# Kernel optimization log

Measured on AMD Instinct MI355X. Metric: run time of the kernel, lower is better.

Reference implementation:

```python
import jax, jax.numpy as jnp
import numpy as np

B, N, D, H, KS, DQ = 2048, 20, 512, 8, 3, 64
DK = D // H
LN_EPS = 1e-5


def _conv1d_same(x_bdn, w_oik):
    # x: [B, D, N], w: [O, I, K] -> [B, O, N], 'same' padding
    return jax.lax.conv_general_dilated(
        x_bdn, w_oik, window_strides=(1,), padding='SAME',
        dimension_numbers=('NCH', 'OIH', 'NCH'))


def _layernorm(x, g, b):
    m = jnp.mean(x, axis=-1, keepdims=True)
    v = jnp.var(x, axis=-1, keepdims=True)
    return (x - m) * jax.lax.rsqrt(v + LN_EPS) * g + b


def setup_inputs() -> dict:
    key = jax.random.key(0)
    ks = jax.random.split(key, 12)
    s = 0.02
    inp = {
        'x': jax.random.normal(ks[0], (B, N, D), dtype=jnp.float32),
        'Wq': jax.random.normal(ks[1], (D, D, KS), dtype=jnp.float32) * s,
        'Wk': jax.random.normal(ks[2], (D, D, KS), dtype=jnp.float32) * s,
        'Wv': jax.random.normal(ks[3], (D, D, KS), dtype=jnp.float32) * s,
        'gq_g': jnp.ones((D,), jnp.float32), 'gq_b': jnp.zeros((D,), jnp.float32),
        'gk_g': jnp.ones((D,), jnp.float32), 'gk_b': jnp.zeros((D,), jnp.float32),
        'gv_g': jnp.ones((D,), jnp.float32), 'gv_b': jnp.zeros((D,), jnp.float32),
        'rel_table': jax.random.normal(ks[4], (2 * N - 1, H), dtype=jnp.float32) * s,
        'gsb': jax.random.normal(ks[5], (H, N, N), dtype=jnp.float32) * s,
        'alpha': jnp.asarray(1.0, jnp.float32),
        'Wqf': jax.random.normal(ks[6], (D, DQ), dtype=jnp.float32) * s,
        'bqf': jnp.zeros((DQ,), jnp.float32),
        'Wqp': jax.random.normal(ks[7], (DQ, H), dtype=jnp.float32) * s,
        'bqp': jnp.zeros((H,), jnp.float32),
        'Wo': jax.random.normal(ks[8], (D, D), dtype=jnp.float32) * s,
        'bo': jnp.zeros((D,), jnp.float32),
    }
    return inp


def reference(x, Wq, Wk, Wv, gq_g, gq_b, gk_g, gk_b, gv_g, gv_b,
              rel_table, gsb, alpha, Wqf, bqf, Wqp, bqp, Wo, bo):
    xp = jnp.transpose(x, (0, 2, 1))  # [B, D, N]
    # conv QKV projections + LayerNorm + residual (use_conv_proj=True path)
    q = x + _layernorm(jnp.transpose(_conv1d_same(xp, Wq), (0, 2, 1)), gq_g, gq_b)
    k = x + _layernorm(jnp.transpose(_conv1d_same(xp, Wk), (0, 2, 1)), gk_g, gk_b)
    v = x + _layernorm(jnp.transpose(_conv1d_same(xp, Wv), (0, 2, 1)), gv_g, gv_b)
    # split heads: [B, H, N, DK]
    q = q.reshape(B, N, H, DK).transpose(0, 2, 1, 3)
    k = k.reshape(B, N, H, DK).transpose(0, 2, 1, 3)
    v = v.reshape(B, N, H, DK).transpose(0, 2, 1, 3)
    scale = 1.0 / jnp.sqrt(jnp.asarray(DK, jnp.float32))
    scores = jnp.einsum('bhnd,bhmd->bhnm', q, k) * scale  # [B, H, N, N]
    # relative positional bias over node index
    idx = jnp.arange(N)[:, None] - jnp.arange(N)[None, :] + N - 1  # [N, N]
    rel_bias = rel_table[idx]  # [N, N, H]
    scores = scores + jnp.transpose(rel_bias, (2, 0, 1))[None]
    # learned global spatial bias
    scores = scores + alpha * gsb[None]
    # dynamic adjacency bias from pairwise node features
    qf = jnp.tanh(x @ Wqf + bqf)  # [B, N, DQ]
    pair = qf[:, :, None, :] - qf[:, None, :, :]  # [B, N, N, DQ]
    dyn = pair @ Wqp + bqp  # [B, N, N, H]
    scores = scores + jnp.transpose(dyn, (0, 3, 1, 2))
    attn = jax.nn.softmax(scores, axis=-1)
    out = jnp.einsum('bhnm,bhmd->bhnd', attn, v)
    out = out.transpose(0, 2, 1, 3).reshape(B, N, D)
    return out @ Wo + bo
```

## Files before the change

kernel.cpp:

```cpp
#include <hip/hip_runtime.h>
#include <stdint.h>

#define Bn   2048
#define Nn   20
#define Dn   512
#define Hn   8
#define Mn   (Bn*Nn)
#define K3n  1536
#define NPn  22
#define BKn  32

typedef __attribute__((ext_vector_type(4))) float  floatx4;
typedef __attribute__((ext_vector_type(8))) __bf16 bf16x8;
typedef __attribute__((ext_vector_type(4))) __bf16 bf16x4;

__device__ __forceinline__ void gload_lds16(const void* g, void* l) {
  __builtin_amdgcn_global_load_lds(
      (const __attribute__((address_space(1))) void*)g,
      (__attribute__((address_space(3))) void*)l, 16, 0, 0);
}

__global__ void k_prep_xpad(const float* __restrict__ x, __bf16* __restrict__ xpad) {
  int idx = blockIdx.x * 256 + threadIdx.x;
  int d8 = idx & 63;
  int t  = idx >> 6;
  if (t >= Bn * NPn) return;
  int n = t % NPn;
  int b = t / NPn;
  bf16x8 v;
  if (n == 0 || n == NPn - 1) {
#pragma unroll
    for (int e = 0; e < 8; ++e) v[e] = (__bf16)0.f;
  } else {
    const float4 x0 = *(const float4*)(x + (size_t)((b * Nn + n - 1) * Dn) + d8 * 8);
    const float4 x1 = *(const float4*)(x + (size_t)((b * Nn + n - 1) * Dn) + d8 * 8 + 4);
    v[0] = (__bf16)x0.x; v[1] = (__bf16)x0.y; v[2] = (__bf16)x0.z; v[3] = (__bf16)x0.w;
    v[4] = (__bf16)x1.x; v[5] = (__bf16)x1.y; v[6] = (__bf16)x1.z; v[7] = (__bf16)x1.w;
  }
  *(bf16x8*)(xpad + (size_t)t * Dn + d8 * 8) = v;
}

__global__ void k_prep_wct(const float* __restrict__ Wq, const float* __restrict__ Wk,
                           const float* __restrict__ Wv, __bf16* __restrict__ wct) {
  int idx = blockIdx.x * 256 + threadIdx.x;
  if (idx >= K3n * K3n) return;
  int kk = idx % K3n;
  int j  = idx / K3n;
  int seg = j >> 9, o = j & 511;
  int kker = kk >> 9, i = kk & 511;
  const float* W = (seg == 0) ? Wq : ((seg == 1) ? Wk : Wv);
  wct[idx] = (__bf16)W[(o * 512 + i) * 3 + kker];
}

__global__ void k_prep_wot(const float* __restrict__ Wo, __bf16* __restrict__ wot) {
  int idx = blockIdx.x * 256 + threadIdx.x;
  if (idx >= Dn * Dn) return;
  int k = idx & 511, c = idx >> 9;
  wot[idx] = (__bf16)Wo[k * Dn + c];
}

__global__ void k_prep_wqft(const float* __restrict__ Wqf, __bf16* __restrict__ wqft) {
  int idx = blockIdx.x * 256 + threadIdx.x;
  if (idx >= Dn * 64) return;
  int d = idx & 511, dq = idx >> 9;
  wqft[idx] = (__bf16)Wqf[d * 64 + dq];
}

__global__ void k_bias(const float* __restrict__ rel, const float* __restrict__ gsb,
                       const float* __restrict__ alpha, const float* __restrict__ bqp,
                       float* __restrict__ bias) {
  int idx = blockIdx.x * 256 + threadIdx.x;
  if (idx >= Hn * Nn * Nn) return;
  int j = idx % Nn;
  int i = (idx / Nn) % Nn;
  int h = idx / (Nn * Nn);
  bias[idx] = rel[(i - j + Nn - 1) * Hn + h] + alpha[0] * gsb[idx] + bqp[h];
}

__global__ __launch_bounds__(512)
void k_qkv(const __bf16* __restrict__ xpad, const __bf16* __restrict__ wct,
           const float* __restrict__ gq_g, const float* __restrict__ gq_b,
           const float* __restrict__ gk_g, const float* __restrict__ gk_b,
           const float* __restrict__ gv_g, const float* __restrict__ gv_b,
           __bf16* __restrict__ qkv) {
  __shared__ __bf16 lA[64 * BKn];
  __shared__ __bf16 lB[512 * BKn];
  __shared__ float red1[256];
  __shared__ float red2[256];

  const int tid  = threadIdx.x;
  const int wave = tid >> 6;
  const int lane = tid & 63;
  const int quad = lane >> 4;
  const int l15  = lane & 15;
  const int rowg = wave >> 2;
  const int colg = wave & 3;

  const int bid   = blockIdx.x;
  const int xcd   = bid & 7;
  const int local = bid >> 3;
  const int seg   = local % 3;
  const int mt    = xcd * 80 + local / 3;
  const int m0    = mt * 64;

  const __bf16* gB[4];
#pragma unroll
  for (int t = 0; t < 4; ++t) {
    int c   = wave * 256 + t * 64 + lane;
    int col = c >> 2;
    int rk  = (c & 3) ^ ((col >> 1) & 3);
    gB[t] = wct + (size_t)(seg * 512 + col) * K3n + rk * 8;
  }
  const __bf16* gA;
  {
    int c   = (wave & 3) * 64 + lane;
    int row = c >> 2;
    int rk  = (c & 3) ^ ((row >> 1) & 3);
    int grow = m0 + row;
    int b = grow / Nn, n = grow - b * Nn;
    gA = xpad + (size_t)(b * NPn + n) * Dn + rk * 8;
  }

  const __bf16* fA[2];
#pragma unroll
  for (int tr = 0; tr < 2; ++tr) {
    int row  = rowg * 32 + tr * 16 + l15;
    int slot = quad ^ ((row >> 1) & 3);
    fA[tr] = lA + row * BKn + slot * 8;
  }
  const __bf16* fB[8];
#pragma unroll
  for (int tc = 0; tc < 8; ++tc) {
    int col  = colg * 128 + tc * 16 + l15;
    int slot = quad ^ ((col >> 1) & 3);
    fB[tc] = lB + col * BKn + slot * 8;
  }

  floatx4 acc[2][8];
  const floatx4 zero = {0.f, 0.f, 0.f, 0.f};
#pragma unroll
  for (int i = 0; i < 2; ++i)
#pragma unroll
    for (int j = 0; j < 8; ++j) acc[i][j] = zero;

  __bf16* dstB = lB + wave * 2048;
  __bf16* dstA = lA + (wave & 3) * 512;

  for (int kt = 0; kt < K3n / BKn; ++kt) {
#pragma unroll
    for (int t = 0; t < 4; ++t) gload_lds16(gB[t], dstB + t * 512);
    if (wave < 4) gload_lds16(gA, dstA);
    __syncthreads();
    bf16x8 a0 = *(const bf16x8*)fA[0];
    bf16x8 a1 = *(const bf16x8*)fA[1];
#pragma unroll
    for (int tc = 0; tc < 8; ++tc) {
      bf16x8 b0 = *(const bf16x8*)fB[tc];
      acc[0][tc] = __builtin_amdgcn_mfma_f32_16x16x32_bf16(a0, b0, acc[0][tc], 0, 0, 0);
      acc[1][tc] = __builtin_amdgcn_mfma_f32_16x16x32_bf16(a1, b0, acc[1][tc], 0, 0, 0);
    }
    __syncthreads();
#pragma unroll
    for (int t = 0; t < 4; ++t) gB[t] += BKn;
    gA += BKn;
  }

  float s1[8], s2[8];
#pragma unroll
  for (int tr = 0; tr < 2; ++tr)
#pragma unroll
    for (int r = 0; r < 4; ++r) {
      float a = 0.f, b2 = 0.f;
#pragma unroll
      for (int tc = 0; tc < 8; ++tc) { float v = acc[tr][tc][r]; a += v; b2 += v * v; }
      s1[tr * 4 + r] = a; s2[tr * 4 + r] = b2;
    }
#pragma unroll
  for (int off = 1; off < 16; off <<= 1)
#pragma unroll
    for (int i = 0; i < 8; ++i) {
      s1[i] += __shfl_xor(s1[i], off, 64);
      s2[i] += __shfl_xor(s2[i], off, 64);
    }
  if (l15 == 0) {
#pragma unroll
    for (int i = 0; i < 8; ++i) {
      int tr = i >> 2, r = i & 3;
      int row = rowg * 32 + tr * 16 + quad * 4 + r;
      red1[row * 4 + colg] = s1[i];
      red2[row * 4 + colg] = s2[i];
    }
  }
  __syncthreads();

  const float* gg = (seg == 0) ? gq_g : ((seg == 1) ? gk_g : gv_g);
  const float* bb = (seg == 0) ? gq_b : ((seg == 1) ? gk_b : gv_b);
#pragma unroll
  for (int tr = 0; tr < 2; ++tr)
#pragma unroll
    for (int r = 0; r < 4; ++r) {
      int row = rowg * 32 + tr * 16 + quad * 4 + r;
      float su = red1[row * 4] + red1[row * 4 + 1] + red1[row * 4 + 2] + red1[row * 4 + 3];
      float sq = red2[row * 4] + red2[row * 4 + 1] + red2[row * 4 + 2] + red2[row * 4 + 3];
      float m  = su * (1.f / 512.f);
      float vv = sq * (1.f / 512.f) - m * m;
      float rstd = rsqrtf(vv + 1e-5f);
      int grow = m0 + row;
      int b = grow / Nn, n2 = grow - b * Nn;
      const __bf16* xr = xpad + (size_t)(b * NPn + n2 + 1) * Dn;
#pragma unroll
      for (int tc = 0; tc < 8; ++tc) {
        int col = colg * 128 + tc * 16 + l15;
        float val = (acc[tr][tc][r] - m) * rstd * gg[col] + bb[col] + (float)xr[col];
        qkv[(size_t)grow * K3n + seg * 512 + col] = (__bf16)val;
      }
    }
}

__global__ __launch_bounds__(256)
void k_qfqp(const __bf16* __restrict__ xpad, const __bf16* __restrict__ wqft,
            const float* __restrict__ bqf, const float* __restrict__ wqp,
            float* __restrict__ qfp) {
  __shared__ __bf16 lA[64 * BKn];
  __shared__ __bf16 lB[64 * BKn];
  __shared__ float lWqpT[8 * 64];
  const int tid  = threadIdx.x;
  const int wave = tid >> 6;
  const int lane = tid & 63;
  const int quad = lane >> 4;
  const int l15  = lane & 15;
  const int m0   = blockIdx.x * 64;

#pragma unroll
  for (int t = tid; t < 512; t += 256) {
    int col = t & 63, h = t >> 6;
    lWqpT[t] = wqp[col * 8 + h];
  }

  int c = wave * 64 + lane;
  int rowc = c >> 2;
  int rk   = (c & 3) ^ ((rowc >> 1) & 3);
  int grow = m0 + rowc;
  int b = grow / Nn, n = grow - b * Nn;
  const __bf16* gA = xpad + (size_t)(b * NPn + n + 1) * Dn + rk * 8;
  const __bf16* gB = wqft + (size_t)rowc * Dn + rk * 8;

  int frow = wave * 16 + l15;
  const __bf16* fA = lA + frow * BKn + (quad ^ ((frow >> 1) & 3)) * 8;
  const __bf16* fB[4];
#pragma unroll
  for (int tc = 0; tc < 4; ++tc) {
    int col = tc * 16 + l15;
    fB[tc] = lB + col * BKn + (quad ^ ((col >> 1) & 3)) * 8;
  }

  const floatx4 zero = {0.f, 0.f, 0.f, 0.f};
  floatx4 acc[4] = {zero, zero, zero, zero};

  for (int kt = 0; kt < Dn / BKn; ++kt) {
    gload_lds16(gA, lA + wave * 512);
    gload_lds16(gB, lB + wave * 512);
    __syncthreads();
    bf16x8 a = *(const bf16x8*)fA;
#pragma unroll
    for (int tc = 0; tc < 4; ++tc)
      acc[tc] = __builtin_amdgcn_mfma_f32_16x16x32_bf16(a, *(const bf16x8*)fB[tc], acc[tc], 0, 0, 0);
    __syncthreads();
    gA += BKn; gB += BKn;
  }

  float part[4][8];
#pragma unroll
  for (int r = 0; r < 4; ++r)
#pragma unroll
    for (int h = 0; h < 8; ++h) part[r][h] = 0.f;
#pragma unroll
  for (int tc = 0; tc < 4; ++tc) {
    int col = tc * 16 + l15;
    float bq = bqf[col];
#pragma unroll
    for (int r = 0; r < 4; ++r) {
      float t = tanhf(acc[tc][r] + bq);
#pragma unroll
      for (int h = 0; h < 8; ++h) part[r][h] += t * lWqpT[h * 64 + col];
    }
  }
#pragma unroll
  for (int off = 1; off < 16; off <<= 1)
#pragma unroll
    for (int r = 0; r < 4; ++r)
#pragma unroll
      for (int h = 0; h < 8; ++h) part[r][h] += __shfl_xor(part[r][h], off, 64);
  if (l15 == 0) {
#pragma unroll
    for (int r = 0; r < 4; ++r) {
      int row = wave * 16 + quad * 4 + r;
#pragma unroll
      for (int h = 0; h < 8; ++h)
        qfp[(size_t)(m0 + row) * 8 + h] = part[r][h];
    }
  }
}

__global__ __launch_bounds__(256)
void k_attn(const __bf16* __restrict__ qkv, const float* __restrict__ qfp,
            const float* __restrict__ bias, __bf16* __restrict__ aout) {
  __shared__ float sq[4][Nn * 64];
  __shared__ float sk[4][Nn * 68];
  __shared__ float sv[4][Nn * 68];
  __shared__ float sp[4][Nn * Nn];
  __shared__ float sf[4][Nn];
  const int tid  = threadIdx.x;
  const int w    = tid >> 6;
  const int lane = tid & 63;
  const int p0 = blockIdx.x * 4 + w;
  const int b = p0 >> 3, h = p0 & 7;
  const __bf16* qb = qkv + (size_t)b * Nn * K3n + h * 64;

  for (int idx = lane; idx < 160; idx += 64) {
    int n = idx >> 3, c = (idx & 7) * 8;
    bf16x8 qv = *(const bf16x8*)(qb + (size_t)n * K3n + c);
    bf16x8 kv = *(const bf16x8*)(qb + (size_t)n * K3n + 512 + c);
    bf16x8 vv = *(const bf16x8*)(qb + (size_t)n * K3n + 1024 + c);
#pragma unroll
    for (int e = 0; e < 8; ++e) {
      sq[w][n * 64 + c + e] = (float)qv[e];
      sk[w][n * 68 + c + e] = (float)kv[e];
      sv[w][n * 68 + c + e] = (float)vv[e];
    }
  }
  if (lane < Nn) sf[w][lane] = qfp[(size_t)(b * Nn + lane) * 8 + h];
  __syncthreads();

  const float* bh = bias + h * Nn * Nn;
  for (int p = lane; p < Nn * Nn; p += 64) {
    int i = p / Nn, j = p - i * Nn;
    const float4* q4 = (const float4*)&sq[w][i * 64];
    const float4* k4 = (const float4*)&sk[w][j * 68];
    float s = 0.f;
#pragma unroll
    for (int d4 = 0; d4 < 16; ++d4) {
      float4 qa = q4[d4], ka = k4[d4];
      s += qa.x * ka.x + qa.y * ka.y + qa.z * ka.z + qa.w * ka.w;
    }
    sp[w][p] = s * 0.125f + bh[p] + sf[w][i] - sf[w][j];
  }
  __syncthreads();
  if (lane < Nn) {
    int i = lane;
    float* row = &sp[w][i * Nn];
    float mx = row[0];
    for (int j = 1; j < Nn; ++j) mx = fmaxf(mx, row[j]);
    float sum = 0.f;
    for (int j = 0; j < Nn; ++j) { float e = __expf(row[j] - mx); row[j] = e; sum += e; }
    float inv = 1.f / sum;
    for (int j = 0; j < Nn; ++j) row[j] *= inv;
  }
  __syncthreads();
  for (int i = 0; i < Nn; ++i) {
    float a = 0.f;
#pragma unroll
    for (int j = 0; j < Nn; ++j) a += sp[w][i * Nn + j] * sv[w][j * 68 + lane];
    aout[(size_t)(b * Nn + i) * Dn + h * 64 + lane] = (__bf16)a;
  }
}

__global__ __launch_bounds__(512)
void k_oproj(const __bf16* __restrict__ aout, const __bf16* __restrict__ wot,
             const float* __restrict__ bo, float* __restrict__ out) {
  __shared__ __bf16 lA[64 * BKn];
  __shared__ __bf16 lB[512 * BKn];
  const int tid  = threadIdx.x;
  const int wave = tid >> 6;
  const int lane = tid & 63;
  const int quad = lane >> 4;
  const int l15  = lane & 15;
  const int rowg = wave >> 2;
  const int colg = wave & 3;
  const int m0   = blockIdx.x * 64;

  const __bf16* gB[4];
#pragma unroll
  for (int t = 0; t < 4; ++t) {
    int c   = wave * 256 + t * 64 + lane;
    int col = c >> 2;
    int rk  = (c & 3) ^ ((col >> 1) & 3);
    gB[t] = wot + (size_t)col * Dn + rk * 8;
  }
  const __bf16* gA;
  {
    int c   = (wave & 3) * 64 + lane;
    int row = c >> 2;
    int rk  = (c & 3) ^ ((row >> 1) & 3);
    gA = aout + (size_t)(m0 + row) * Dn + rk * 8;
  }
  const __bf16* fA[2];
#pragma unroll
  for (int tr = 0; tr < 2; ++tr) {
    int row = rowg * 32 + tr * 16 + l15;
    fA[tr] = lA + row * BKn + (quad ^ ((row >> 1) & 3)) * 8;
  }
  const __bf16* fB[8];
#pragma unroll
  for (int tc = 0; tc < 8; ++tc) {
    int col = colg * 128 + tc * 16 + l15;
    fB[tc] = lB + col * BKn + (quad ^ ((col >> 1) & 3)) * 8;
  }

  const floatx4 zero = {0.f, 0.f, 0.f, 0.f};
  floatx4 acc[2][8];
#pragma unroll
  for (int i = 0; i < 2; ++i)
#pragma unroll
    for (int j = 0; j < 8; ++j) acc[i][j] = zero;

  __bf16* dstB = lB + wave * 2048;
  __bf16* dstA = lA + (wave & 3) * 512;

  for (int kt = 0; kt < Dn / BKn; ++kt) {
#pragma unroll
    for (int t = 0; t < 4; ++t) gload_lds16(gB[t], dstB + t * 512);
    if (wave < 4) gload_lds16(gA, dstA);
    __syncthreads();
    bf16x8 a0 = *(const bf16x8*)fA[0];
    bf16x8 a1 = *(const bf16x8*)fA[1];
#pragma unroll
    for (int tc = 0; tc < 8; ++tc) {
      bf16x8 b0 = *(const bf16x8*)fB[tc];
      acc[0][tc] = __builtin_amdgcn_mfma_f32_16x16x32_bf16(a0, b0, acc[0][tc], 0, 0, 0);
      acc[1][tc] = __builtin_amdgcn_mfma_f32_16x16x32_bf16(a1, b0, acc[1][tc], 0, 0, 0);
    }
    __syncthreads();
#pragma unroll
    for (int t = 0; t < 4; ++t) gB[t] += BKn;
    gA += BKn;
  }
#pragma unroll
  for (int tr = 0; tr < 2; ++tr)
#pragma unroll
    for (int r = 0; r < 4; ++r) {
      int row = rowg * 32 + tr * 16 + quad * 4 + r;
#pragma unroll
      for (int tc = 0; tc < 8; ++tc) {
        int col = colg * 128 + tc * 16 + l15;
        out[(size_t)(m0 + row) * Dn + col] = acc[tr][tc][r] + bo[col];
      }
    }
}

static const size_t OFF_XPAD = 0;
static const size_t OFF_WCT  = 46137344;
static const size_t OFF_WOT  = 50855936;
static const size_t OFF_WQFT = 51380224;
static const size_t OFF_QKV  = 51445760;
static const size_t OFF_QFP  = 177274880;
static const size_t OFF_BIAS = 178585600;
static const size_t OFF_AOUT = 0;

extern "C" void kernel_launch(void* const* d_in, const int* in_sizes, int n_in,
                              void* d_out, int out_size, void* d_ws, size_t ws_size,
                              hipStream_t stream) {
  (void)in_sizes; (void)n_in; (void)out_size; (void)ws_size;
  const float* x     = (const float*)d_in[0];
  const float* Wq    = (const float*)d_in[1];
  const float* Wk    = (const float*)d_in[2];
  const float* Wv    = (const float*)d_in[3];
  const float* gq_g  = (const float*)d_in[4];
  const float* gq_b  = (const float*)d_in[5];
  const float* gk_g  = (const float*)d_in[6];
  const float* gk_b  = (const float*)d_in[7];
  const float* gv_g  = (const float*)d_in[8];
  const float* gv_b  = (const float*)d_in[9];
  const float* rel   = (const float*)d_in[10];
  const float* gsb   = (const float*)d_in[11];
  const float* alpha = (const float*)d_in[12];
  const float* Wqf   = (const float*)d_in[13];
  const float* bqf   = (const float*)d_in[14];
  const float* Wqp   = (const float*)d_in[15];
  const float* bqp   = (const float*)d_in[16];
  const float* Wo    = (const float*)d_in[17];
  const float* bo    = (const float*)d_in[18];
  float* out = (float*)d_out;
  char* ws = (char*)d_ws;

  __bf16* xpad = (__bf16*)(ws + OFF_XPAD);
  __bf16* wct  = (__bf16*)(ws + OFF_WCT);
  __bf16* wot  = (__bf16*)(ws + OFF_WOT);
  __bf16* wqft = (__bf16*)(ws + OFF_WQFT);
  __bf16* qkv  = (__bf16*)(ws + OFF_QKV);
  float*  qfp  = (float*)(ws + OFF_QFP);
  float*  bias = (float*)(ws + OFF_BIAS);
  __bf16* aout = (__bf16*)(ws + OFF_AOUT);

  k_prep_xpad<<<(Bn * NPn * (Dn / 8) + 255) / 256, 256, 0, stream>>>(x, xpad);
  k_prep_wct <<<(K3n * K3n + 255) / 256, 256, 0, stream>>>(Wq, Wk, Wv, wct);
  k_prep_wot <<<(Dn * Dn + 255) / 256, 256, 0, stream>>>(Wo, wot);
  k_prep_wqft<<<(Dn * 64 + 255) / 256, 256, 0, stream>>>(Wqf, wqft);
  k_bias     <<<(Hn * Nn * Nn + 255) / 256, 256, 0, stream>>>(rel, gsb, alpha, bqp, bias);

  k_qkv <<<Mn / 64 * 3, 512, 0, stream>>>(xpad, wct, gq_g, gq_b, gk_g, gk_b, gv_g, gv_b, qkv);
  k_qfqp<<<Mn / 64, 256, 0, stream>>>(xpad, wqft, bqf, Wqp, qfp);
  k_attn<<<(Bn * Hn) / 4, 256, 0, stream>>>(qkv, qfp, bias, aout);
  k_oproj<<<Mn / 64, 512, 0, stream>>>(aout, wot, bo, out);
}
```

Measured before the change: 651.4 us.

## Triple-buffer QKV GEMM loads and double the M tile to 128

The fused conv-QKV GEMM now uses a 128-row M tile (4x8 MFMA tiles per wave), which halves the number of blocks and the redundant weight traffic per output row. It replaces the load/sync/compute loop with a three-stage LDS ring, so global-to-LDS loads for stage k+2 are issued before computing stage k, waited on with explicit vmcnt counters, and only one barrier per step remains. It also raises MFMA wave priority and asks for 2 blocks per CU via launch bounds. The costs are more LDS (about 120KB) and 128 accumulator registers per lane, which could limit occupancy or cause spills.

```diff
diff --git a/kernel.cpp b/kernel.cpp
--- a/kernel.cpp
+++ b/kernel.cpp
@@ -77,16 +77,15 @@
   bias[idx] = rel[(i - j + Nn - 1) * Hn + h] + alpha[0] * gsb[idx] + bqp[h];
 }
 
-__global__ __launch_bounds__(512)
+__global__ __launch_bounds__(512, 2)
 void k_qkv(const __bf16* __restrict__ xpad, const __bf16* __restrict__ wct,
            const float* __restrict__ gq_g, const float* __restrict__ gq_b,
            const float* __restrict__ gk_g, const float* __restrict__ gk_b,
            const float* __restrict__ gv_g, const float* __restrict__ gv_b,
            __bf16* __restrict__ qkv) {
-  __shared__ __bf16 lA[64 * BKn];
-  __shared__ __bf16 lB[512 * BKn];
-  __shared__ float red1[256];
-  __shared__ float red2[256];
+  __shared__ __bf16 lds[3 * 20480];
+  __shared__ float red1[512];
+  __shared__ float red2[512];
 
   const int tid  = threadIdx.x;
   const int wave = tid >> 6;
@@ -100,20 +99,24 @@
   const int xcd   = bid & 7;
   const int local = bid >> 3;
   const int seg   = local % 3;
-  const int mt    = xcd * 80 + local / 3;
-  const int m0    = mt * 64;
-
-  const __bf16* gB[4];
-#pragma unroll
-  for (int t = 0; t < 4; ++t) {
-    int c   = wave * 256 + t * 64 + lane;
-    int col = c >> 2;
-    int rk  = (c & 3) ^ ((col >> 1) & 3);
-    gB[t] = wct + (size_t)(seg * 512 + col) * K3n + rk * 8;
+  const int mt    = xcd * 40 + local / 3;
+  const int m0    = mt * 128;
+
+  const __bf16 *gB0, *gB1, *gB2, *gB3;
+  {
+    int c, col, rk;
+    c = wave * 256 + 0 * 64 + lane; col = c >> 2; rk = (c & 3) ^ ((col >> 1) & 3);
+    gB0 = wct + (size_t)(seg * 512 + col) * K3n + rk * 8;
+    c = wave * 256 + 1 * 64 + lane; col = c >> 2; rk = (c & 3) ^ ((col >> 1) & 3);
+    gB1 = wct + (size_t)(seg * 512 + col) * K3n + rk * 8;
+    c = wave * 256 + 2 * 64 + lane; col = c >> 2; rk = (c & 3) ^ ((col >> 1) & 3);
+    gB2 = wct + (size_t)(seg * 512 + col) * K3n + rk * 8;
+    c = wave * 256 + 3 * 64 + lane; col = c >> 2; rk = (c & 3) ^ ((col >> 1) & 3);
+    gB3 = wct + (size_t)(seg * 512 + col) * K3n + rk * 8;
   }
   const __bf16* gA;
   {
-    int c   = (wave & 3) * 64 + lane;
+    int c   = tid;
     int row = c >> 2;
     int rk  = (c & 3) ^ ((row >> 1) & 3);
     int grow = m0 + row;
@@ -121,72 +124,98 @@
     gA = xpad + (size_t)(b * NPn + n) * Dn + rk * 8;
   }
 
-  const __bf16* fA[2];
-#pragma unroll
-  for (int tr = 0; tr < 2; ++tr) {
-    int row  = rowg * 32 + tr * 16 + l15;
-    int slot = quad ^ ((row >> 1) & 3);
-    fA[tr] = lA + row * BKn + slot * 8;
-  }
-  const __bf16* fB[8];
-#pragma unroll
-  for (int tc = 0; tc < 8; ++tc) {
-    int col  = colg * 128 + tc * 16 + l15;
-    int slot = quad ^ ((col >> 1) & 3);
-    fB[tc] = lB + col * BKn + slot * 8;
-  }
-
-  floatx4 acc[2][8];
+  int fAo0, fAo1, fAo2, fAo3, fBo[8];
+  {
+    int row;
+    row = rowg * 64 + 0 * 16 + l15; fAo0 = row * BKn + (quad ^ ((row >> 1) & 3)) * 8;
+    row = rowg * 64 + 1 * 16 + l15; fAo1 = row * BKn + (quad ^ ((row >> 1) & 3)) * 8;
+    row = rowg * 64 + 2 * 16 + l15; fAo2 = row * BKn + (quad ^ ((row >> 1) & 3)) * 8;
+    row = rowg * 64 + 3 * 16 + l15; fAo3 = row * BKn + (quad ^ ((row >> 1) & 3)) * 8;
+#pragma unroll
+    for (int tc = 0; tc < 8; ++tc) {
+      int col = colg * 128 + tc * 16 + l15;
+      fBo[tc] = 4096 + col * BKn + (quad ^ ((col >> 1) & 3)) * 8;
+    }
+  }
+
+  const int dA = wave * 512;
+  const int dB = 4096 + wave * 2048;
+
+  floatx4 acc[4][8];
   const floatx4 zero = {0.f, 0.f, 0.f, 0.f};
 #pragma unroll
-  for (int i = 0; i < 2; ++i)
+  for (int i = 0; i < 4; ++i)
 #pragma unroll
     for (int j = 0; j < 8; ++j) acc[i][j] = zero;
 
-  __bf16* dstB = lB + wave * 2048;
-  __bf16* dstA = lA + (wave & 3) * 512;
-
-  for (int kt = 0; kt < K3n / BKn; ++kt) {
-#pragma unroll
-    for (int t = 0; t < 4; ++t) gload_lds16(gB[t], dstB + t * 512);
-    if (wave < 4) gload_lds16(gA, dstA);
-    __syncthreads();
-    bf16x8 a0 = *(const bf16x8*)fA[0];
-    bf16x8 a1 = *(const bf16x8*)fA[1];
-#pragma unroll
-    for (int tc = 0; tc < 8; ++tc) {
-      bf16x8 b0 = *(const bf16x8*)fB[tc];
-      acc[0][tc] = __builtin_amdgcn_mfma_f32_16x16x32_bf16(a0, b0, acc[0][tc], 0, 0, 0);
-      acc[1][tc] = __builtin_amdgcn_mfma_f32_16x16x32_bf16(a1, b0, acc[1][tc], 0, 0, 0);
-    }
-    __syncthreads();
-#pragma unroll
-    for (int t = 0; t < 4; ++t) gB[t] += BKn;
-    gA += BKn;
-  }
-
-  float s1[8], s2[8];
-#pragma unroll
-  for (int tr = 0; tr < 2; ++tr)
+#define QKV_STAGE(NB) do {                                             \
+    __bf16* _s = lds + (NB) * 20480;                                   \
+    gload_lds16(gA,  _s + dA);          gA  += BKn;                    \
+    gload_lds16(gB0, _s + dB);          gB0 += BKn;                    \
+    gload_lds16(gB1, _s + dB + 512);    gB1 += BKn;                    \
+    gload_lds16(gB2, _s + dB + 1024);   gB2 += BKn;                    \
+    gload_lds16(gB3, _s + dB + 1536);   gB3 += BKn;                    \
+  } while (0)
+
+#define QKV_STEP(CB, NB, DOSTAGE, VMS) do {                            \
+    if (DOSTAGE) QKV_STAGE(NB);                                        \
+    const __bf16* _L = lds + (CB) * 20480;                             \
+    bf16x8 _a0 = *(const bf16x8*)(_L + fAo0);                          \
+    bf16x8 _a1 = *(const bf16x8*)(_L + fAo1);                          \
+    bf16x8 _a2 = *(const bf16x8*)(_L + fAo2);                          \
+    bf16x8 _a3 = *(const bf16x8*)(_L + fAo3);                          \
+    __builtin_amdgcn_s_setprio(1);                                     \
+    _Pragma("unroll")                                                  \
+    for (int _n = 0; _n < 8; ++_n) {                                   \
+      bf16x8 _b = *(const bf16x8*)(_L + fBo[_n]);                      \
+      acc[0][_n] = __builtin_amdgcn_mfma_f32_16x16x32_bf16(_a0, _b, acc[0][_n], 0, 0, 0); \
+      acc[1][_n] = __builtin_amdgcn_mfma_f32_16x16x32_bf16(_a1, _b, acc[1][_n], 0, 0, 0); \
+      acc[2][_n] = __builtin_amdgcn_mfma_f32_16x16x32_bf16(_a2, _b, acc[2][_n], 0, 0, 0); \
+      acc[3][_n] = __builtin_amdgcn_mfma_f32_16x16x32_bf16(_a3, _b, acc[3][_n], 0, 0, 0); \
+    }                                                                  \
+    __builtin_amdgcn_s_setprio(0);                                     \
+    asm volatile("s_waitcnt vmcnt(" VMS ") lgkmcnt(0)\n\ts_barrier" ::: "memory"); \
+  } while (0)
+
+  QKV_STAGE(0);
+  QKV_STAGE(1);
+  asm volatile("s_waitcnt vmcnt(5)\n\ts_barrier" ::: "memory");
+
+#pragma unroll 1
+  for (int it = 0; it < 15; ++it) {
+    QKV_STEP(0, 2, true, "5");
+    QKV_STEP(1, 0, true, "5");
+    QKV_STEP(2, 1, true, "5");
+  }
+  QKV_STEP(0, 2, true, "5");
+  QKV_STEP(1, 0, false, "0");
+  QKV_STEP(2, 0, false, "0");
+
+#undef QKV_STEP
+#undef QKV_STAGE
+
+  float s1[16], s2[16];
+#pragma unroll
+  for (int m = 0; m < 4; ++m)
 #pragma unroll
     for (int r = 0; r < 4; ++r) {
       float a = 0.f, b2 = 0.f;
 #pragma unroll
-      for (int tc = 0; tc < 8; ++tc) { float v = acc[tr][tc][r]; a += v; b2 += v * v; }
-      s1[tr * 4 + r] = a; s2[tr * 4 + r] = b2;
+      for (int n = 0; n < 8; ++n) { float v = acc[m][n][r]; a += v; b2 += v * v; }
+      s1[m * 4 + r] = a; s2[m * 4 + r] = b2;
     }
 #pragma unroll
   for (int off = 1; off < 16; off <<= 1)
 #pragma unroll
-    for (int i = 0; i < 8; ++i) {
+    for (int i = 0; i < 16; ++i) {
       s1[i] += __shfl_xor(s1[i], off, 64);
       s2[i] += __shfl_xor(s2[i], off, 64);
     }
   if (l15 == 0) {
 #pragma unroll
-    for (int i = 0; i < 8; ++i) {
-      int tr = i >> 2, r = i & 3;
-      int row = rowg * 32 + tr * 16 + quad * 4 + r;
+    for (int i = 0; i < 16; ++i) {
+      int m = i >> 2, r = i & 3;
+      int row = rowg * 64 + m * 16 + quad * 4 + r;
       red1[row * 4 + colg] = s1[i];
       red2[row * 4 + colg] = s2[i];
     }
@@ -196,22 +225,22 @@
   const float* gg = (seg == 0) ? gq_g : ((seg == 1) ? gk_g : gv_g);
   const float* bb = (seg == 0) ? gq_b : ((seg == 1) ? gk_b : gv_b);
 #pragma unroll
-  for (int tr = 0; tr < 2; ++tr)
+  for (int m = 0; m < 4; ++m)
 #pragma unroll
     for (int r = 0; r < 4; ++r) {
-      int row = rowg * 32 + tr * 16 + quad * 4 + r;
+      int row = rowg * 64 + m * 16 + quad * 4 + r;
       float su = red1[row * 4] + red1[row * 4 + 1] + red1[row * 4 + 2] + red1[row * 4 + 3];
       float sq = red2[row * 4] + red2[row * 4 + 1] + red2[row * 4 + 2] + red2[row * 4 + 3];
-      float m  = su * (1.f / 512.f);
-      float vv = sq * (1.f / 512.f) - m * m;
+      float mn = su * (1.f / 512.f);
+      float vv = sq * (1.f / 512.f) - mn * mn;
       float rstd = rsqrtf(vv + 1e-5f);
       int grow = m0 + row;
       int b = grow / Nn, n2 = grow - b * Nn;
       const __bf16* xr = xpad + (size_t)(b * NPn + n2 + 1) * Dn;
 #pragma unroll
-      for (int tc = 0; tc < 8; ++tc) {
-        int col = colg * 128 + tc * 16 + l15;
-        float val = (acc[tr][tc][r] - m) * rstd * gg[col] + bb[col] + (float)xr[col];
+      for (int n = 0; n < 8; ++n) {
+        int col = colg * 128 + n * 16 + l15;
+        float val = (acc[m][n][r] - mn) * rstd * gg[col] + bb[col] + (float)xr[col];
         qkv[(size_t)grow * K3n + seg * 512 + col] = (__bf16)val;
       }
     }
@@ -498,7 +527,7 @@
   k_prep_wqft<<<(Dn * 64 + 255) / 256, 256, 0, stream>>>(Wqf, wqft);
   k_bias     <<<(Hn * Nn * Nn + 255) / 256, 256, 0, stream>>>(rel, gsb, alpha, bqp, bias);
 
-  k_qkv <<<Mn / 64 * 3, 512, 0, stream>>>(xpad, wct, gq_g, gq_b, gk_g, gk_b, gv_g, gv_b, qkv);
+  k_qkv <<<Mn / 128 * 3, 512, 0, stream>>>(xpad, wct, gq_g, gq_b, gk_g, gk_b, gv_g, gv_b, qkv);
   k_qfqp<<<Mn / 64, 256, 0, stream>>>(xpad, wqft, bqf, Wqp, qfp);
   k_attn<<<(Bn * Hn) / 4, 256, 0, stream>>>(qkv, qfp, bias, aout);
   k_oproj<<<Mn / 64, 512, 0, stream>>>(aout, wot, bo, out);
```

Result: faster. 593.5 us (-8.9%).

## Restructure QKV and output GEMMs with register-held pre-fragmented weights and double buffering

Applied to the files above, without the earlier changes.

Weights are pre-packed into MFMA fragment order so each wave loads its B operands straight into registers instead of staging them through shared memory. Each block shrinks to 4 waves, each owning a 64x128 tile. The A tile is double-buffered per wave in LDS and the next k-step is prefetched during the MFMAs. Block barriers inside the K loop are removed and s_setprio is raised around the MFMA sequences. The trade-off is much higher register pressure (64 accumulators plus two B fragment sets), every wave redundantly loading the A tile, and a changed block-to-segment mapping that affects L2 reuse.

```diff
diff --git a/kernel.cpp b/kernel.cpp
--- a/kernel.cpp
+++ b/kernel.cpp
@@ -40,23 +40,38 @@
   *(bf16x8*)(xpad + (size_t)t * Dn + d8 * 8) = v;
 }
 
-__global__ void k_prep_wct(const float* __restrict__ Wq, const float* __restrict__ Wk,
-                           const float* __restrict__ Wv, __bf16* __restrict__ wct) {
-  int idx = blockIdx.x * 256 + threadIdx.x;
-  if (idx >= K3n * K3n) return;
-  int kk = idx % K3n;
-  int j  = idx / K3n;
-  int seg = j >> 9, o = j & 511;
-  int kker = kk >> 9, i = kk & 511;
+__global__ void k_prep_wctf(const float* __restrict__ Wq, const float* __restrict__ Wk,
+                            const float* __restrict__ Wv, __bf16* __restrict__ wctf) {
+  int t = blockIdx.x * 256 + threadIdx.x;
+  if (t >= 48 * 96 * 64) return;
+  int l  = t & 63;
+  int cb = (t >> 6) % 96;
+  int kt = t / (96 * 64);
+  int col = cb * 16 + (l & 15);
+  int k   = kt * 32 + (l >> 4) * 8;
+  int seg = col >> 9, o = col & 511;
+  int kker = k >> 9, i = k & 511;
   const float* W = (seg == 0) ? Wq : ((seg == 1) ? Wk : Wv);
-  wct[idx] = (__bf16)W[(o * 512 + i) * 3 + kker];
-}
-
-__global__ void k_prep_wot(const float* __restrict__ Wo, __bf16* __restrict__ wot) {
-  int idx = blockIdx.x * 256 + threadIdx.x;
-  if (idx >= Dn * Dn) return;
-  int k = idx & 511, c = idx >> 9;
-  wot[idx] = (__bf16)Wo[k * Dn + c];
+  const float* s = W + ((size_t)o * 512 + i) * 3 + kker;
+  bf16x8 v;
+#pragma unroll
+  for (int e = 0; e < 8; ++e) v[e] = (__bf16)s[e * 3];
+  *(bf16x8*)(wctf + (size_t)t * 8) = v;
+}
+
+__global__ void k_prep_wotf(const float* __restrict__ Wo, __bf16* __restrict__ wotf) {
+  int t = blockIdx.x * 256 + threadIdx.x;
+  if (t >= 16 * 32 * 64) return;
+  int l  = t & 63;
+  int cb = (t >> 6) & 31;
+  int kt = t / (32 * 64);
+  int col = cb * 16 + (l & 15);
+  int k   = kt * 32 + (l >> 4) * 8;
+  const float* s = Wo + (size_t)k * 512 + col;
+  bf16x8 v;
+#pragma unroll
+  for (int e = 0; e < 8; ++e) v[e] = (__bf16)s[(size_t)e * 512];
+  *(bf16x8*)(wotf + (size_t)t * 8) = v;
 }
 
 __global__ void k_prep_wqft(const float* __restrict__ Wqf, __bf16* __restrict__ wqft) {
@@ -77,118 +92,132 @@
   bias[idx] = rel[(i - j + Nn - 1) * Hn + h] + alpha[0] * gsb[idx] + bqp[h];
 }
 
-__global__ __launch_bounds__(512)
-void k_qkv(const __bf16* __restrict__ xpad, const __bf16* __restrict__ wct,
+#define LOADB(DST, ADV) do {                                           \
+    _Pragma("unroll")                                                  \
+    for (int _tc = 0; _tc < 8; ++_tc)                                  \
+      DST[_tc] = *(const bf16x8*)(gW + _tc * 512);                     \
+    gW += (ADV);                                                       \
+  } while (0)
+
+#define STAGEA(NB) do {                                                \
+    gload_lds16(gA0, myA + (NB) * 2048 +    0); gA0 += BKn;            \
+    gload_lds16(gA1, myA + (NB) * 2048 +  512); gA1 += BKn;            \
+    gload_lds16(gA2, myA + (NB) * 2048 + 1024); gA2 += BKn;            \
+    gload_lds16(gA3, myA + (NB) * 2048 + 1536); gA3 += BKn;            \
+  } while (0)
+
+#define GSTEP(KT, CUR, NXT, CB, NB, LASTKT, ADV) do {                  \
+    const __bf16* _L = myA + (CB) * 2048;                              \
+    bf16x8 _a0 = *(const bf16x8*)(_L + fAo[0]);                        \
+    bf16x8 _a1 = *(const bf16x8*)(_L + fAo[1]);                        \
+    bf16x8 _a2 = *(const bf16x8*)(_L + fAo[2]);                        \
+    bf16x8 _a3 = *(const bf16x8*)(_L + fAo[3]);                        \
+    if ((KT) < (LASTKT)) { LOADB(NXT, ADV); STAGEA(NB); }              \
+    __builtin_amdgcn_s_setprio(1);                                     \
+    _Pragma("unroll")                                                  \
+    for (int _tc = 0; _tc < 8; ++_tc) {                                \
+      acc[0][_tc] = __builtin_amdgcn_mfma_f32_16x16x32_bf16(_a0, CUR[_tc], acc[0][_tc], 0, 0, 0); \
+      acc[1][_tc] = __builtin_amdgcn_mfma_f32_16x16x32_bf16(_a1, CUR[_tc], acc[1][_tc], 0, 0, 0); \
+      acc[2][_tc] = __builtin_amdgcn_mfma_f32_16x16x32_bf16(_a2, CUR[_tc], acc[2][_tc], 0, 0, 0); \
+      acc[3][_tc] = __builtin_amdgcn_mfma_f32_16x16x32_bf16(_a3, CUR[_tc], acc[3][_tc], 0, 0, 0); \
+    }                                                                  \
+    __builtin_amdgcn_s_setprio(0);                                     \
+    asm volatile("s_waitcnt vmcnt(0)" ::: "memory");                   \
+  } while (0)
+
+__global__ __launch_bounds__(256, 2)
+void k_qkv(const __bf16* __restrict__ xpad, const __bf16* __restrict__ wctf,
            const float* __restrict__ gq_g, const float* __restrict__ gq_b,
            const float* __restrict__ gk_g, const float* __restrict__ gk_b,
            const float* __restrict__ gv_g, const float* __restrict__ gv_b,
            __bf16* __restrict__ qkv) {
-  __shared__ __bf16 lA[64 * BKn];
-  __shared__ __bf16 lB[512 * BKn];
+  __shared__ __bf16 lA[4][2][2048];
   __shared__ float red1[256];
   __shared__ float red2[256];
 
   const int tid  = threadIdx.x;
-  const int wave = tid >> 6;
+  const int wv   = tid >> 6;
   const int lane = tid & 63;
   const int quad = lane >> 4;
   const int l15  = lane & 15;
-  const int rowg = wave >> 2;
-  const int colg = wave & 3;
 
   const int bid   = blockIdx.x;
   const int xcd   = bid & 7;
   const int local = bid >> 3;
-  const int seg   = local % 3;
-  const int mt    = xcd * 80 + local / 3;
+  const int seg   = local / 80;
+  const int mt    = xcd * 80 + (local % 80);
   const int m0    = mt * 64;
 
-  const __bf16* gB[4];
-#pragma unroll
-  for (int t = 0; t < 4; ++t) {
-    int c   = wave * 256 + t * 64 + lane;
-    int col = c >> 2;
-    int rk  = (c & 3) ^ ((col >> 1) & 3);
-    gB[t] = wct + (size_t)(seg * 512 + col) * K3n + rk * 8;
-  }
-  const __bf16* gA;
+  const __bf16 *gA0, *gA1, *gA2, *gA3;
   {
-    int c   = (wave & 3) * 64 + lane;
-    int row = c >> 2;
-    int rk  = (c & 3) ^ ((row >> 1) & 3);
-    int grow = m0 + row;
-    int b = grow / Nn, n = grow - b * Nn;
-    gA = xpad + (size_t)(b * NPn + n) * Dn + rk * 8;
-  }
-
-  const __bf16* fA[2];
-#pragma unroll
-  for (int tr = 0; tr < 2; ++tr) {
-    int row  = rowg * 32 + tr * 16 + l15;
-    int slot = quad ^ ((row >> 1) & 3);
-    fA[tr] = lA + row * BKn + slot * 8;
-  }
-  const __bf16* fB[8];
-#pragma unroll
-  for (int tc = 0; tc < 8; ++tc) {
-    int col  = colg * 128 + tc * 16 + l15;
-    int slot = quad ^ ((col >> 1) & 3);
-    fB[tc] = lB + col * BKn + slot * 8;
-  }
-
-  floatx4 acc[2][8];
+    int c, row, rk, grow, b, n;
+    c = 0 * 64 + lane; row = c >> 2; rk = (c & 3) ^ ((row >> 1) & 3);
+    grow = m0 + row; b = grow / Nn; n = grow - b * Nn;
+    gA0 = xpad + (size_t)(b * NPn + n) * Dn + rk * 8;
+    c = 1 * 64 + lane; row = c >> 2; rk = (c & 3) ^ ((row >> 1) & 3);
+    grow = m0 + row; b = grow / Nn; n = grow - b * Nn;
+    gA1 = xpad + (size_t)(b * NPn + n) * Dn + rk * 8;
+    c = 2 * 64 + lane; row = c >> 2; rk = (c & 3) ^ ((row >> 1) & 3);
+    grow = m0 + row; b = grow / Nn; n = grow - b * Nn;
+    gA2 = xpad + (size_t)(b * NPn + n) * Dn + rk * 8;
+    c = 3 * 64 + lane; row = c >> 2; rk = (c & 3) ^ ((row >> 1) & 3);
+    grow = m0 + row; b = grow / Nn; n = grow - b * Nn;
+    gA3 = xpad + (size_t)(b * NPn + n) * Dn + rk * 8;
+  }
+
+  const __bf16* gW = wctf + ((size_t)(seg * 32 + wv * 8) * 512) + lane * 8;
+
+  int fAo[4];
+#pragma unroll
+  for (int mi = 0; mi < 4; ++mi) {
+    int row = mi * 16 + l15;
+    fAo[mi] = row * BKn + (quad ^ ((row >> 1) & 3)) * 8;
+  }
+  __bf16* myA = &lA[wv][0][0];
+
+  floatx4 acc[4][8];
   const floatx4 zero = {0.f, 0.f, 0.f, 0.f};
 #pragma unroll
-  for (int i = 0; i < 2; ++i)
+  for (int i = 0; i < 4; ++i)
 #pragma unroll
     for (int j = 0; j < 8; ++j) acc[i][j] = zero;
 
-  __bf16* dstB = lB + wave * 2048;
-  __bf16* dstA = lA + (wave & 3) * 512;
-
-  for (int kt = 0; kt < K3n / BKn; ++kt) {
-#pragma unroll
-    for (int t = 0; t < 4; ++t) gload_lds16(gB[t], dstB + t * 512);
-    if (wave < 4) gload_lds16(gA, dstA);
-    __syncthreads();
-    bf16x8 a0 = *(const bf16x8*)fA[0];
-    bf16x8 a1 = *(const bf16x8*)fA[1];
-#pragma unroll
-    for (int tc = 0; tc < 8; ++tc) {
-      bf16x8 b0 = *(const bf16x8*)fB[tc];
-      acc[0][tc] = __builtin_amdgcn_mfma_f32_16x16x32_bf16(a0, b0, acc[0][tc], 0, 0, 0);
-      acc[1][tc] = __builtin_amdgcn_mfma_f32_16x16x32_bf16(a1, b0, acc[1][tc], 0, 0, 0);
-    }
-    __syncthreads();
-#pragma unroll
-    for (int t = 0; t < 4; ++t) gB[t] += BKn;
-    gA += BKn;
-  }
-
-  float s1[8], s2[8];
-#pragma unroll
-  for (int tr = 0; tr < 2; ++tr)
+  bf16x8 bA[8], bB[8];
+
+  STAGEA(0);
+  LOADB(bA, 49152);
+  asm volatile("s_waitcnt vmcnt(0)" ::: "memory");
+
+#pragma unroll 1
+  for (int it = 0; it < 24; ++it) {
+    GSTEP(2 * it,     bA, bB, 0, 1, 47, 49152);
+    GSTEP(2 * it + 1, bB, bA, 1, 0, 47, 49152);
+  }
+
+  float s1[16], s2[16];
+#pragma unroll
+  for (int mi = 0; mi < 4; ++mi)
 #pragma unroll
     for (int r = 0; r < 4; ++r) {
       float a = 0.f, b2 = 0.f;
 #pragma unroll
-      for (int tc = 0; tc < 8; ++tc) { float v = acc[tr][tc][r]; a += v; b2 += v * v; }
-      s1[tr * 4 + r] = a; s2[tr * 4 + r] = b2;
+      for (int tc = 0; tc < 8; ++tc) { float v = acc[mi][tc][r]; a += v; b2 += v * v; }
+      s1[mi * 4 + r] = a; s2[mi * 4 + r] = b2;
     }
 #pragma unroll
   for (int off = 1; off < 16; off <<= 1)
 #pragma unroll
-    for (int i = 0; i < 8; ++i) {
+    for (int i = 0; i < 16; ++i) {
       s1[i] += __shfl_xor(s1[i], off, 64);
       s2[i] += __shfl_xor(s2[i], off, 64);
     }
   if (l15 == 0) {
 #pragma unroll
-    for (int i = 0; i < 8; ++i) {
-      int tr = i >> 2, r = i & 3;
-      int row = rowg * 32 + tr * 16 + quad * 4 + r;
-      red1[row * 4 + colg] = s1[i];
-      red2[row * 4 + colg] = s2[i];
+    for (int i = 0; i < 16; ++i) {
+      int mi = i >> 2, r = i & 3;
+      int row = mi * 16 + quad * 4 + r;
+      red1[row * 4 + wv] = s1[i];
+      red2[row * 4 + wv] = s2[i];
     }
   }
   __syncthreads();
@@ -196,22 +225,22 @@
   const float* gg = (seg == 0) ? gq_g : ((seg == 1) ? gk_g : gv_g);
   const float* bb = (seg == 0) ? gq_b : ((seg == 1) ? gk_b : gv_b);
 #pragma unroll
-  for (int tr = 0; tr < 2; ++tr)
+  for (int mi = 0; mi < 4; ++mi)
 #pragma unroll
     for (int r = 0; r < 4; ++r) {
-      int row = rowg * 32 + tr * 16 + quad * 4 + r;
+      int row = mi * 16 + quad * 4 + r;
       float su = red1[row * 4] + red1[row * 4 + 1] + red1[row * 4 + 2] + red1[row * 4 + 3];
       float sq = red2[row * 4] + red2[row * 4 + 1] + red2[row * 4 + 2] + red2[row * 4 + 3];
-      float m  = su * (1.f / 512.f);
-      float vv = sq * (1.f / 512.f) - m * m;
+      float mn = su * (1.f / 512.f);
+      float vv = sq * (1.f / 512.f) - mn * mn;
       float rstd = rsqrtf(vv + 1e-5f);
       int grow = m0 + row;
       int b = grow / Nn, n2 = grow - b * Nn;
       const __bf16* xr = xpad + (size_t)(b * NPn + n2 + 1) * Dn;
 #pragma unroll
       for (int tc = 0; tc < 8; ++tc) {
-        int col = colg * 128 + tc * 16 + l15;
-        float val = (acc[tr][tc][r] - m) * rstd * gg[col] + bb[col] + (float)xr[col];
+        int col = wv * 128 + tc * 16 + l15;
+        float val = (acc[mi][tc][r] - mn) * rstd * gg[col] + bb[col] + (float)xr[col];
         qkv[(size_t)grow * K3n + seg * 512 + col] = (__bf16)val;
       }
     }
@@ -221,8 +250,8 @@
 void k_qfqp(const __bf16* __restrict__ xpad, const __bf16* __restrict__ wqft,
             const float* __restrict__ bqf, const float* __restrict__ wqp,
             float* __restrict__ qfp) {
-  __shared__ __bf16 lA[64 * BKn];
-  __shared__ __bf16 lB[64 * BKn];
+  __shared__ __bf16 sA[64 * BKn];
+  __shared__ __bf16 sB[64 * BKn];
   __shared__ float lWqpT[8 * 64];
   const int tid  = threadIdx.x;
   const int wave = tid >> 6;
@@ -246,20 +275,20 @@
   const __bf16* gB = wqft + (size_t)rowc * Dn + rk * 8;
 
   int frow = wave * 16 + l15;
-  const __bf16* fA = lA + frow * BKn + (quad ^ ((frow >> 1) & 3)) * 8;
+  const __bf16* fA = sA + frow * BKn + (quad ^ ((frow >> 1) & 3)) * 8;
   const __bf16* fB[4];
 #pragma unroll
   for (int tc = 0; tc < 4; ++tc) {
     int col = tc * 16 + l15;
-    fB[tc] = lB + col * BKn + (quad ^ ((col >> 1) & 3)) * 8;
+    fB[tc] = sB + col * BKn + (quad ^ ((col >> 1) & 3)) * 8;
   }
 
   const floatx4 zero = {0.f, 0.f, 0.f, 0.f};
   floatx4 acc[4] = {zero, zero, zero, zero};
 
   for (int kt = 0; kt < Dn / BKn; ++kt) {
-    gload_lds16(gA, lA + wave * 512);
-    gload_lds16(gB, lB + wave * 512);
+    gload_lds16(gA, sA + wave * 512);
+    gload_lds16(gB, sB + wave * 512);
     __syncthreads();
     bf16x8 a = *(const bf16x8*)fA;
 #pragma unroll
@@ -365,85 +394,69 @@
   }
 }
 
-__global__ __launch_bounds__(512)
-void k_oproj(const __bf16* __restrict__ aout, const __bf16* __restrict__ wot,
+__global__ __launch_bounds__(256, 2)
+void k_oproj(const __bf16* __restrict__ aout, const __bf16* __restrict__ wotf,
              const float* __restrict__ bo, float* __restrict__ out) {
-  __shared__ __bf16 lA[64 * BKn];
-  __shared__ __bf16 lB[512 * BKn];
+  __shared__ __bf16 lA[4][2][2048];
   const int tid  = threadIdx.x;
-  const int wave = tid >> 6;
+  const int wv   = tid >> 6;
   const int lane = tid & 63;
   const int quad = lane >> 4;
   const int l15  = lane & 15;
-  const int rowg = wave >> 2;
-  const int colg = wave & 3;
-  const int m0   = blockIdx.x * 64;
-
-  const __bf16* gB[4];
-#pragma unroll
-  for (int t = 0; t < 4; ++t) {
-    int c   = wave * 256 + t * 64 + lane;
-    int col = c >> 2;
-    int rk  = (c & 3) ^ ((col >> 1) & 3);
-    gB[t] = wot + (size_t)col * Dn + rk * 8;
-  }
-  const __bf16* gA;
+
+  const int bid = blockIdx.x;
+  const int m0  = ((bid & 7) * 80 + (bid >> 3)) * 64;
+
+  const __bf16 *gA0, *gA1, *gA2, *gA3;
   {
-    int c   = (wave & 3) * 64 + lane;
-    int row = c >> 2;
-    int rk  = (c & 3) ^ ((row >> 1) & 3);
-    gA = aout + (size_t)(m0 + row) * Dn + rk * 8;
-  }
-  const __bf16* fA[2];
-#pragma unroll
-  for (int tr = 0; tr < 2; ++tr) {
-    int row = rowg * 32 + tr * 16 + l15;
-    fA[tr] = lA + row * BKn + (quad ^ ((row >> 1) & 3)) * 8;
-  }
-  const __bf16* fB[8];
-#pragma unroll
-  for (int tc = 0; tc < 8; ++tc) {
-    int col = colg * 128 + tc * 16 + l15;
-    fB[tc] = lB + col * BKn + (quad ^ ((col >> 1) & 3)) * 8;
-  }
-
+    int c, row, rk;
+    c = 0 * 64 + lane; row = c >> 2; rk = (c & 3) ^ ((row >> 1) & 3);
+    gA0 = aout + (size_t)(m0 + row) * Dn + rk * 8;
+    c = 1 * 64 + lane; row = c >> 2; rk = (c & 3) ^ ((row >> 1) & 3);
+    gA1 = aout + (size_t)(m0 + row) * Dn + rk * 8;
+    c = 2 * 64 + lane; row = c >> 2; rk = (c & 3) ^ ((row >> 1) & 3);
+    gA2 = aout + (size_t)(m0 + row) * Dn + rk * 8;
+    c = 3 * 64 + lane; row = c >> 2; rk = (c & 3) ^ ((row >> 1) & 3);
+    gA3 = aout + (size_t)(m0 + row) * Dn + rk * 8;
+  }
+  const __bf16* gW = wotf + ((size_t)(wv * 8) * 512) + lane * 8;
+
+  int fAo[4];
+#pragma unroll
+  for (int mi = 0; mi < 4; ++mi) {
+    int row = mi * 16 + l15;
+    fAo[mi] = row * BKn + (quad ^ ((row >> 1) & 3)) * 8;
+  }
+  __bf16* myA = &lA[wv][0][0];
+
+  floatx4 acc[4][8];
   const floatx4 zero = {0.f, 0.f, 0.f, 0.f};
-  floatx4 acc[2][8];
-#pragma unroll
-  for (int i = 0; i < 2; ++i)
+#pragma unroll
+  for (int i = 0; i < 4; ++i)
 #pragma unroll
     for (int j = 0; j < 8; ++j) acc[i][j] = zero;
 
-  __bf16* dstB = lB + wave * 2048;
-  __bf16* dstA = lA + (wave & 3) * 512;
-
-  for (int kt = 0; kt < Dn / BKn; ++kt) {
-#pragma unroll
-    for (int t = 0; t < 4; ++t) gload_lds16(gB[t], dstB + t * 512);
-    if (wave < 4) gload_lds16(gA, dstA);
-    __syncthreads();
-    bf16x8 a0 = *(const bf16x8*)fA[0];
-    bf16x8 a1 = *(const bf16x8*)fA[1];
-#pragma unroll
-    for (int tc = 0; tc < 8; ++tc) {
-      bf16x8 b0 = *(const bf16x8*)fB[tc];
-      acc[0][tc] = __builtin_amdgcn_mfma_f32_16x16x32_bf16(a0, b0, acc[0][tc], 0, 0, 0);
-      acc[1][tc] = __builtin_amdgcn_mfma_f32_16x16x32_bf16(a1, b0, acc[1][tc], 0, 0, 0);
-    }
-    __syncthreads();
-#pragma unroll
-    for (int t = 0; t < 4; ++t) gB[t] += BKn;
-    gA += BKn;
-  }
-#pragma unroll
-  for (int tr = 0; tr < 2; ++tr)
+  bf16x8 bA[8], bB[8];
+
+  STAGEA(0);
+  LOADB(bA, 16384);
+  asm volatile("s_waitcnt vmcnt(0)" ::: "memory");
+
+#pragma unroll 1
+  for (int it = 0; it < 8; ++it) {
+    GSTEP(2 * it,     bA, bB, 0, 1, 15, 16384);
+    GSTEP(2 * it + 1, bB, bA, 1, 0, 15, 16384);
+  }
+
+#pragma unroll
+  for (int mi = 0; mi < 4; ++mi)
 #pragma unroll
     for (int r = 0; r < 4; ++r) {
-      int row = rowg * 32 + tr * 16 + quad * 4 + r;
+      int row = mi * 16 + quad * 4 + r;
 #pragma unroll
       for (int tc = 0; tc < 8; ++tc) {
-        int col = colg * 128 + tc * 16 + l15;
-        out[(size_t)(m0 + row) * Dn + col] = acc[tr][tc][r] + bo[col];
+        int col = wv * 128 + tc * 16 + l15;
+        out[(size_t)(m0 + row) * Dn + col] = acc[mi][tc][r] + bo[col];
       }
     }
 }
@@ -484,8 +497,8 @@
   char* ws = (char*)d_ws;
 
   __bf16* xpad = (__bf16*)(ws + OFF_XPAD);
-  __bf16* wct  = (__bf16*)(ws + OFF_WCT);
-  __bf16* wot  = (__bf16*)(ws + OFF_WOT);
+  __bf16* wctf = (__bf16*)(ws + OFF_WCT);
+  __bf16* wotf = (__bf16*)(ws + OFF_WOT);
   __bf16* wqft = (__bf16*)(ws + OFF_WQFT);
   __bf16* qkv  = (__bf16*)(ws + OFF_QKV);
   float*  qfp  = (float*)(ws + OFF_QFP);
@@ -493,13 +506,13 @@
   __bf16* aout = (__bf16*)(ws + OFF_AOUT);
 
   k_prep_xpad<<<(Bn * NPn * (Dn / 8) + 255) / 256, 256, 0, stream>>>(x, xpad);
-  k_prep_wct <<<(K3n * K3n + 255) / 256, 256, 0, stream>>>(Wq, Wk, Wv, wct);
-  k_prep_wot <<<(Dn * Dn + 255) / 256, 256, 0, stream>>>(Wo, wot);
+  k_prep_wctf<<<(48 * 96 * 64 + 255) / 256, 256, 0, stream>>>(Wq, Wk, Wv, wctf);
+  k_prep_wotf<<<(16 * 32 * 64 + 255) / 256, 256, 0, stream>>>(Wo, wotf);
   k_prep_wqft<<<(Dn * 64 + 255) / 256, 256, 0, stream>>>(Wqf, wqft);
   k_bias     <<<(Hn * Nn * Nn + 255) / 256, 256, 0, stream>>>(rel, gsb, alpha, bqp, bias);
 
-  k_qkv <<<Mn / 64 * 3, 512, 0, stream>>>(xpad, wct, gq_g, gq_b, gk_g, gk_b, gv_g, gv_b, qkv);
+  k_qkv <<<Mn / 64 * 3, 256, 0, stream>>>(xpad, wctf, gq_g, gq_b, gk_g, gk_b, gv_g, gv_b, qkv);
   k_qfqp<<<Mn / 64, 256, 0, stream>>>(xpad, wqft, bqf, Wqp, qfp);
   k_attn<<<(Bn * Hn) / 4, 256, 0, stream>>>(qkv, qfp, bias, aout);
-  k_oproj<<<Mn / 64, 512, 0, stream>>>(aout, wot, bo, out);
-}
+  k_oproj<<<Mn / 64, 256, 0, stream>>>(aout, wotf, bo, out);
+}
```

After: 569.7 us. 12.5% less time.
